# Performance work log

Measured on AMD Instinct MI355X. Metric: run time of the kernel, lower is better.

The kernel has to match this reference:

```python
import jax, jax.numpy as jnp
import numpy as np

P = 16      # patch size
D = 768     # d_model
H = 12      # heads
L = 12      # layers
F = 3072    # d_ff
NC = 1000   # num classes
B = 32
IMG = 224
S = (IMG // P) ** 2 + 1  # 197 tokens (CLS + patches)
EPS = 1e-5


def layernorm(x, s, b):
    m = jnp.mean(x, axis=-1, keepdims=True)
    v = jnp.var(x, axis=-1, keepdims=True)
    return (x - m) * jax.lax.rsqrt(v + EPS) * s + b


def setup_inputs() -> dict:
    key = jax.random.key(0)
    ks = jax.random.split(key, 16)
    sd = 0.02
    patch_dim = P * P * 3  # 768
    inp = {
        "img": jax.random.normal(ks[0], (B, 3, IMG, IMG), jnp.float32),
        "proj_w": jax.random.normal(ks[1], (patch_dim, D), jnp.float32) * sd,
        "proj_b": jnp.zeros((D,), jnp.float32),
        "cls_token": jax.random.normal(ks[2], (1, 1, D), jnp.float32) * sd,
        "pos_emb": jax.random.normal(ks[3], (1, S, D), jnp.float32) * sd,
        # stacked per-layer params [L, ...]
        "ln1_s": jnp.ones((L, D), jnp.float32),
        "ln1_b": jnp.zeros((L, D), jnp.float32),
        "wq": jax.random.normal(ks[4], (L, D, D), jnp.float32) * sd,
        "bq": jnp.zeros((L, D), jnp.float32),
        "wk": jax.random.normal(ks[5], (L, D, D), jnp.float32) * sd,
        "bk": jnp.zeros((L, D), jnp.float32),
        "wv": jax.random.normal(ks[6], (L, D, D), jnp.float32) * sd,
        "bv": jnp.zeros((L, D), jnp.float32),
        "wo": jax.random.normal(ks[7], (L, D, D), jnp.float32) * sd,
        "bo": jnp.zeros((L, D), jnp.float32),
        "ln2_s": jnp.ones((L, D), jnp.float32),
        "ln2_b": jnp.zeros((L, D), jnp.float32),
        "w1": jax.random.normal(ks[8], (L, D, F), jnp.float32) * sd,
        "b1": jnp.zeros((L, F), jnp.float32),
        "w2": jax.random.normal(ks[9], (L, F, D), jnp.float32) * sd,
        "b2": jnp.zeros((L, D), jnp.float32),
        "fnorm_s": jnp.ones((D,), jnp.float32),
        "fnorm_b": jnp.zeros((D,), jnp.float32),
        "head_w": jax.random.normal(ks[10], (D, NC), jnp.float32) * sd,
        "head_b": jnp.zeros((NC,), jnp.float32),
    }
    return inp


def vit_forward(img, proj_w, proj_b, cls_token, pos_emb, ln1_s, ln1_b,
                wq, bq, wk, bk, wv, bv, wo, bo, ln2_s, ln2_b,
                w1, b1, w2, b2, fnorm_s, fnorm_b, head_w, head_b):
    b = img.shape[0]
    g = IMG // P
    # rearrange 'b c (h ph) (w pw) -> b (h w) (ph pw c)'
    x = img.reshape(b, 3, g, P, g, P)
    x = x.transpose(0, 2, 4, 3, 5, 1).reshape(b, g * g, P * P * 3)
    x = x @ proj_w + proj_b                      # [b, 196, D]
    cls = jnp.broadcast_to(cls_token, (b, 1, D))
    x = jnp.concatenate([cls, x], axis=1)        # [b, 197, D]
    x = x + pos_emb                              # learnable positional encoding

    dk = D // H
    scale = 1.0 / jnp.sqrt(jnp.float32(dk))

    def layer(x, p):
        (l1s, l1b, Wq, Bq, Wk, Bk, Wv, Bv, Wo, Bo,
         l2s, l2b, W1, B1, W2, B2) = p
        # pre-norm self-attention with residual
        xn = layernorm(x, l1s, l1b)
        q = (xn @ Wq + Bq).reshape(b, S, H, dk)
        k = (xn @ Wk + Bk).reshape(b, S, H, dk)
        v = (xn @ Wv + Bv).reshape(b, S, H, dk)
        scores = jnp.einsum('bqhd,bkhd->bhqk', q, k) * scale
        attn = jax.nn.softmax(scores, axis=-1)
        ao = jnp.einsum('bhqk,bkhd->bqhd', attn, v).reshape(b, S, D)
        x = x + (ao @ Wo + Bo)
        # pre-norm FFN with residual
        xn = layernorm(x, l2s, l2b)
        h = jax.nn.gelu(xn @ W1 + B1, approximate=False)
        x = x + (h @ W2 + B2)
        return x, None

    params = (ln1_s, ln1_b, wq, bq, wk, bk, wv, bv, wo, bo,
              ln2_s, ln2_b, w1, b1, w2, b2)
    x, _ = jax.lax.scan(layer, x, params)
    x = layernorm(x, fnorm_s, fnorm_b)
    cls_out = x[:, 0, :]
    return cls_out @ head_w + head_b             # [b, num_classes]


def reference(img, proj_w, proj_b, cls_token, pos_emb, ln1_s, ln1_b,
              wq, bq, wk, bk, wv, bv, wo, bo, ln2_s, ln2_b,
              w1, b1, w2, b2, fnorm_s, fnorm_b, head_w, head_b):
    return vit_forward(img, proj_w, proj_b, cls_token, pos_emb, ln1_s, ln1_b,
                       wq, bq, wk, bk, wv, bv, wo, bo, ln2_s, ln2_b,
                       w1, b1, w2, b2, fnorm_s, fnorm_b, head_w, head_b)
```

## Files before the change

kernel.cpp:

```cpp
#include <hip/hip_runtime.h>
#include <stdint.h>

typedef __attribute__((ext_vector_type(4))) float  f32x4;
typedef __attribute__((ext_vector_type(8))) _Float16 f16x8;
typedef __attribute__((ext_vector_type(8))) unsigned short u16x8;

__device__ __forceinline__ unsigned short f2h(float f) {
    _Float16 h = (_Float16)f;
    union { _Float16 h; unsigned short u; } cv; cv.h = h; return cv.u;
}

__device__ __forceinline__ f32x4 mfma16(f16x8 a, f16x8 b, f32x4 c) {
    return __builtin_amdgcn_mfma_f32_16x16x32_f16(a, b, c, 0, 0, 0);
}

__device__ __forceinline__ void async16(const unsigned short* g, unsigned short* l) {
    __builtin_amdgcn_global_load_lds(
        (const __attribute__((address_space(1))) unsigned int*)g,
        (__attribute__((address_space(3))) unsigned int*)l,
        16, 0, 0);
}

template<int EPI, int BK>
__global__ __launch_bounds__(256, (BK == 32 ? 4 : 3))
void gemm_k(const unsigned short* __restrict__ A, const unsigned short* __restrict__ Bw,
            int M, int K, int N,
            float* __restrict__ p0, unsigned short* __restrict__ p1,
            const float* __restrict__ p2, const float* __restrict__ p3,
            unsigned short* __restrict__ p4, unsigned short* __restrict__ p5)
{
    __shared__ unsigned short smem[2 * 64 * BK + 2 * 128 * BK];
    unsigned short (*lA)[64 * BK]  = (unsigned short(*)[64 * BK])smem;
    unsigned short (*lB)[128 * BK] = (unsigned short(*)[128 * BK])(smem + 2 * 64 * BK);
    const int tid  = threadIdx.x;
    const int lane = tid & 63;
    const int wid  = tid >> 6;

    const int gx  = gridDim.x;
    const int nwg = gx * gridDim.y;
    const int lin = blockIdx.y * gx + blockIdx.x;
    const int q = nwg >> 3, r = nwg & 7;
    const int xcd = lin & 7, i = lin >> 3;
    const int wg  = (xcd < r ? xcd * (q + 1) : r * (q + 1) + (xcd - r) * q) + i;
    const int m0 = (wg / gx) * 64;
    const int n0 = (wg % gx) * 128;

    const int colBase = wid * 32;
    const int fr = lane & 15, fg = lane >> 4;

    f32x4 acc[4][2];
#pragma unroll
    for (int a = 0; a < 4; ++a)
#pragma unroll
        for (int b = 0; b < 2; ++b) acc[a][b] = (f32x4){0.f, 0.f, 0.f, 0.f};

    const int nk = K / BK;
    constexpr int CPR = BK / 8;
    constexpr int ACH = 64 * CPR;
    constexpr int NH  = (ACH + 128 * CPR) / 256;

    auto stage = [&](int buf, int kt) {
        const int k0 = kt * BK;
#pragma unroll
        for (int h = 0; h < NH; ++h) {
            const int c = h * 256 + tid;
            const int wbase = h * 256 + wid * 64;
            if (c < ACH) {
                const int row = c / CPR, kc = c % CPR;
                const int gkc = (BK == 32) ? (kc ^ ((row >> 1) & 3)) : (kc ^ (row & 7));
                int ar = m0 + row; if (ar > M - 1) ar = M - 1;
                async16(A + (size_t)ar * K + k0 + gkc * 8,
                        &lA[buf][(size_t)wbase * 8]);
            } else {
                const int cb = c - ACH;
                const int row = cb / CPR, kc = cb % CPR;
                const int gkc = (BK == 32) ? (kc ^ ((row >> 1) & 3)) : (kc ^ (row & 7));
                async16(Bw + (size_t)(n0 + row) * K + k0 + gkc * 8,
                        &lB[buf][(size_t)(wbase - ACH) * 8]);
            }
        }
    };

    stage(0, 0);
    for (int kt = 0; kt < nk; ++kt) {
        __syncthreads();
        if (kt + 1 < nk) stage((kt + 1) & 1, kt + 1);
        const int buf = kt & 1;
#pragma unroll
        for (int kk = 0; kk < BK / 32; ++kk) {
            f16x8 af[4], bfv[2];
#pragma unroll
            for (int mi = 0; mi < 4; ++mi) {
                int row = mi * 16 + fr;
                int pc  = (BK == 32) ? (fg ^ ((row >> 1) & 3))
                                     : ((kk * 4 + fg) ^ (row & 7));
                af[mi] = *(const f16x8*)(&lA[buf][row * BK + pc * 8]);
            }
#pragma unroll
            for (int ni = 0; ni < 2; ++ni) {
                int row = colBase + ni * 16 + fr;
                int pc  = (BK == 32) ? (fg ^ ((row >> 1) & 3))
                                     : ((kk * 4 + fg) ^ (row & 7));
                bfv[ni] = *(const f16x8*)(&lB[buf][row * BK + pc * 8]);
            }
#pragma unroll
            for (int mi = 0; mi < 4; ++mi)
#pragma unroll
                for (int ni = 0; ni < 2; ++ni)
                    acc[mi][ni] = mfma16(af[mi], bfv[ni], acc[mi][ni]);
        }
    }

    const int mat0 = (EPI == 0) ? (n0 / 768) : 0;

    if constexpr (EPI == 0 || EPI == 2) {
        if (EPI == 2 || mat0 < 2) {
            unsigned short* sm = smem;
            __syncthreads();
#pragma unroll
            for (int mi = 0; mi < 4; ++mi)
#pragma unroll
                for (int ni = 0; ni < 2; ++ni) {
                    const int lcol = colBase + ni * 16 + fr;
                    const int colg = n0 + lcol;
#pragma unroll
                    for (int reg = 0; reg < 4; ++reg) {
                        const int lrow = mi * 16 + fg * 4 + reg;
                        float val = acc[mi][ni][reg] + p2[colg];
                        if (EPI == 2)
                            val = 0.5f * val * (1.0f + erff(val * 0.70710678118654752f));
                        sm[lrow * 128 + lcol] = f2h(val);
                    }
                }
            __syncthreads();
#pragma unroll
            for (int it = 0; it < 4; ++it) {
                const int e = it * 256 + tid;
                const int lrow = e >> 4, cch = e & 15;
                const int grow = m0 + lrow;
                if (grow >= M) continue;
                const u16x8 v = *(const u16x8*)(&sm[lrow * 128 + cch * 8]);
                if (EPI == 2) {
                    *(u16x8*)(p1 + (size_t)grow * 3072 + n0 + cch * 8) = v;
                } else {
                    const int colg = n0 + cch * 8;
                    const int w = colg - mat0 * 768;
                    const int h = w >> 6, d = w & 63;
                    const int b = grow / 197, s = grow - b * 197;
                    unsigned short* dst = (mat0 == 0) ? p1 : p4;
                    *(u16x8*)(dst + ((((size_t)b * 12 + h) * 197 + s) * 64 + d)) = v;
                }
            }
        } else {
#pragma unroll
            for (int mi = 0; mi < 4; ++mi)
#pragma unroll
                for (int ni = 0; ni < 2; ++ni) {
                    const int col = n0 + colBase + ni * 16 + fr;
                    const int w = col - 1536;
                    const int h = w >> 6, d = w & 63;
#pragma unroll
                    for (int reg = 0; reg < 4; ++reg) {
                        const int row = m0 + mi * 16 + fg * 4 + reg;
                        if (row >= M) continue;
                        const int b = row / 197, s = row - b * 197;
                        float val = acc[mi][ni][reg] + p2[col];
                        p5[(((size_t)b * 12 + h) * 64 + d) * 208 + s] = f2h(val);
                    }
                }
        }
    } else {
#pragma unroll
        for (int mi = 0; mi < 4; ++mi) {
#pragma unroll
            for (int ni = 0; ni < 2; ++ni) {
                const int col = n0 + colBase + ni * 16 + fr;
#pragma unroll
                for (int reg = 0; reg < 4; ++reg) {
                    const int row = m0 + mi * 16 + fg * 4 + reg;
                    if (row >= M) continue;
                    const float v = acc[mi][ni][reg];
                    if constexpr (EPI == 1 || EPI == 3) {
                        size_t idx = (size_t)row * 768 + col;
                        p0[idx] = p0[idx] + v + p2[col];
                    } else {
                        int b = row / 196, p = row - b * 196;
                        float val = v + p2[col] + p3[(size_t)(1 + p) * 768 + col];
                        p0[((size_t)(b * 197 + 1 + p)) * 768 + col] = val;
                    }
                }
            }
        }
    }
}

__device__ __forceinline__ void convT_body(const float* __restrict__ src,
                                           unsigned short* __restrict__ dst,
                                           int K, int N, int bx, int by,
                                           float (*t)[65])
{
    const int tid = threadIdx.x;
    const int n0 = bx * 64, k0 = by * 64;
    int r = tid >> 4, cq = tid & 15;
#pragma unroll
    for (int i = 0; i < 4; ++i) {
        f32x4 v = *(const f32x4*)(src + (size_t)(k0 + r + i * 16) * N + n0 + cq * 4);
        t[r + i * 16][cq * 4 + 0] = v.x;
        t[r + i * 16][cq * 4 + 1] = v.y;
        t[r + i * 16][cq * 4 + 2] = v.z;
        t[r + i * 16][cq * 4 + 3] = v.w;
    }
    __syncthreads();
    int nl = tid >> 2, kq = tid & 3;
    u16x8 o0, o1;
#pragma unroll
    for (int j = 0; j < 8; ++j) {
        o0[j] = f2h(t[kq * 16 + j][nl]);
        o1[j] = f2h(t[kq * 16 + 8 + j][nl]);
    }
    unsigned short* d = dst + (size_t)(n0 + nl) * K + k0 + kq * 16;
    *(u16x8*)(d)     = o0;
    *(u16x8*)(d + 8) = o1;
}

__device__ __forceinline__ void prep_block(int pid,
            const float* __restrict__ wq, const float* __restrict__ wk,
            const float* __restrict__ wv, const float* __restrict__ wo,
            const float* __restrict__ w1, const float* __restrict__ w2,
            const float* __restrict__ bq, const float* __restrict__ bk,
            const float* __restrict__ bv,
            unsigned short* __restrict__ wqkvT, unsigned short* __restrict__ woT,
            unsigned short* __restrict__ w1T, unsigned short* __restrict__ w2T,
            float* __restrict__ bqkv, float (*t)[65])
{
    if (pid == 1728) {
        for (int c = threadIdx.x; c < 2304; c += 256) {
            int m = c / 768, w = c - m * 768;
            bqkv[c] = (m == 0) ? bq[w] : (m == 1 ? bk[w] : bv[w]);
        }
        return;
    }
    const float* src; unsigned short* dst; int K, N, bx, by;
    if (pid < 576) {
        int mat = pid / 144, r = pid - mat * 144;
        K = 768; N = 768; bx = r % 12; by = r / 12;
        if (mat == 0)      { src = wq; dst = wqkvT; }
        else if (mat == 1) { src = wk; dst = wqkvT + 768ull * 768; }
        else if (mat == 2) { src = wv; dst = wqkvT + 1536ull * 768; }
        else               { src = wo; dst = woT; }
    } else if (pid < 1152) {
        int r = pid - 576; K = 768; N = 3072; bx = r % 48; by = r / 48;
        src = w1; dst = w1T;
    } else {
        int r = pid - 1152; K = 3072; N = 768; bx = r % 12; by = r / 12;
        src = w2; dst = w2T;
    }
    convT_body(src, dst, K, N, bx, by, t);
}

__global__ __launch_bounds__(256)
void prep_k(const float* __restrict__ wq, const float* __restrict__ wk,
            const float* __restrict__ wv, const float* __restrict__ wo,
            const float* __restrict__ w1, const float* __restrict__ w2,
            const float* __restrict__ bq, const float* __restrict__ bk,
            const float* __restrict__ bv,
            unsigned short* __restrict__ wqkvT, unsigned short* __restrict__ woT,
            unsigned short* __restrict__ w1T, unsigned short* __restrict__ w2T,
            float* __restrict__ bqkv)
{
    __shared__ float t[64][65];
    prep_block(blockIdx.x, wq, wk, wv, wo, w1, w2, bq, bk, bv,
               wqkvT, woT, w1T, w2T, bqkv, t);
}

__global__ __launch_bounds__(256, 4)
void attn_prep_k(const unsigned short* __restrict__ qb, const unsigned short* __restrict__ kb,
                 const unsigned short* __restrict__ vt, unsigned short* __restrict__ ao,
                 const float* __restrict__ wq, const float* __restrict__ wk,
                 const float* __restrict__ wv, const float* __restrict__ wo,
                 const float* __restrict__ w1, const float* __restrict__ w2,
                 const float* __restrict__ bq, const float* __restrict__ bk,
                 const float* __restrict__ bv,
                 unsigned short* __restrict__ wqkvT, unsigned short* __restrict__ woT,
                 unsigned short* __restrict__ w1T, unsigned short* __restrict__ w2T,
                 float* __restrict__ bqkv)
{
    __shared__ float smbuf[32 * 210 + 32];

    const int bid = blockIdx.x;
    if (bid >= 2688) {
        prep_block(bid - 2688, wq, wk, wv, wo, w1, w2, bq, bk, bv,
                   wqkvT, woT, w1T, w2T, bqkv,
                   reinterpret_cast<float(*)[65]>(smbuf));
        return;
    }

    float* sc   = smbuf;
    float* rinv = smbuf + 32 * 210;

    const int bh = bid % 384;
    const int qt = bid / 384;
    const int b = bh / 12, h = bh - b * 12;
    const unsigned short* qh  = qb + (size_t)bh * 197 * 64;
    const unsigned short* kh  = kb + (size_t)bh * 197 * 64;
    const unsigned short* vth = vt + (size_t)bh * 64 * 208;
    const int tid = threadIdx.x, lane = tid & 63, wid = tid >> 6;
    const int fr = lane & 15, fg = lane >> 4;

    f16x8 qf[2][2];
#pragma unroll
    for (int mi = 0; mi < 2; ++mi)
#pragma unroll
        for (int kc = 0; kc < 2; ++kc) {
            int s = qt * 32 + mi * 16 + fr; if (s > 196) s = 196;
            qf[mi][kc] = *(const f16x8*)(qh + (size_t)s * 64 + kc * 32 + fg * 8);
        }

    for (int nt = wid; nt < 13; nt += 4) {
        f32x4 a0 = (f32x4){0.f,0.f,0.f,0.f}, a1 = a0;
        int rs = nt * 16 + fr; if (rs > 196) rs = 196;
#pragma unroll
        for (int kc = 0; kc < 2; ++kc) {
            f16x8 kf = *(const f16x8*)(kh + (size_t)rs * 64 + kc * 32 + fg * 8);
            a0 = mfma16(qf[0][kc], kf, a0);
            a1 = mfma16(qf[1][kc], kf, a1);
        }
        int ccol = nt * 16 + fr;
        bool valid = (ccol < 197);
#pragma unroll
        for (int reg = 0; reg < 4; ++reg) {
            int mr = fg * 4 + reg;
            sc[mr * 210 + ccol]        = valid ? a0[reg] * 0.125f : -1e30f;
            sc[(16 + mr) * 210 + ccol] = valid ? a1[reg] * 0.125f : -1e30f;
        }
    }
    __syncthreads();

    {
        int row = tid >> 3, j = tid & 7;
        float m = -1e30f;
        for (int c = j; c < 208; c += 8) m = fmaxf(m, sc[row * 210 + c]);
#pragma unroll
        for (int o = 1; o < 8; o <<= 1) m = fmaxf(m, __shfl_xor(m, o));
        float sum = 0.f;
        for (int c = j; c < 208; c += 8) {
            float e = __expf(sc[row * 210 + c] - m);
            sc[row * 210 + c] = e;
            sum += e;
        }
#pragma unroll
        for (int o = 1; o < 8; o <<= 1) sum += __shfl_xor(sum, o);
        if (j == 0) rinv[row] = 1.0f / sum;
    }
    __syncthreads();

    f32x4 o0 = (f32x4){0.f,0.f,0.f,0.f}, o1 = o0;
    const int dbase = wid * 16;
    for (int kt = 0; kt < 7; ++kt) {
        int kb8 = kt * 32 + fg * 8;
        f16x8 pa0, pa1, vf;
        if (kb8 >= 208) {
#pragma unroll
            for (int j = 0; j < 8; ++j) { pa0[j] = (_Float16)0.f; pa1[j] = (_Float16)0.f; vf[j] = (_Float16)0.f; }
        } else {
            const float* pr0 = &sc[fr * 210 + kb8];
            const float* pr1 = &sc[(16 + fr) * 210 + kb8];
#pragma unroll
            for (int j = 0; j < 8; ++j) { pa0[j] = (_Float16)pr0[j]; pa1[j] = (_Float16)pr1[j]; }
            vf = *(const f16x8*)(vth + (size_t)(dbase + fr) * 208 + kb8);
        }
        o0 = mfma16(pa0, vf, o0);
        o1 = mfma16(pa1, vf, o1);
    }
#pragma unroll
    for (int reg = 0; reg < 4; ++reg) {
        int mr0 = fg * 4 + reg, s0 = qt * 32 + mr0;
        if (s0 < 197)
            ao[((size_t)(b * 197 + s0)) * 768 + h * 64 + dbase + fr] = f2h(o0[reg] * rinv[mr0]);
        int mr1 = 16 + fg * 4 + reg, s1 = qt * 32 + mr1;
        if (s1 < 197)
            ao[((size_t)(b * 197 + s1)) * 768 + h * 64 + dbase + fr] = f2h(o1[reg] * rinv[mr1]);
    }
}

__global__ __launch_bounds__(256, 4)
void ln_k(const float* __restrict__ x, const float* __restrict__ gs,
          const float* __restrict__ gb, unsigned short* __restrict__ out)
{
    const int row = blockIdx.x;
    const int tid = threadIdx.x, lane = tid & 63, wid = tid >> 6;
    const float* xr = x + (size_t)row * 768;
    float v0 = xr[tid], v1 = xr[tid + 256], v2 = xr[tid + 512];
    float s = v0 + v1 + v2;
    float q = v0 * v0 + v1 * v1 + v2 * v2;
#pragma unroll
    for (int o = 1; o < 64; o <<= 1) { s += __shfl_xor(s, o); q += __shfl_xor(q, o); }
    __shared__ float ws[4], wq[4];
    if (lane == 0) { ws[wid] = s; wq[wid] = q; }
    __syncthreads();
    s = ws[0] + ws[1] + ws[2] + ws[3];
    q = wq[0] + wq[1] + wq[2] + wq[3];
    const float mean = s * (1.0f / 768.0f);
    const float rstd = rsqrtf(q * (1.0f / 768.0f) - mean * mean + 1e-5f);
    unsigned short* orow = out + (size_t)row * 768;
    orow[tid]       = f2h((v0 - mean) * rstd * gs[tid]       + gb[tid]);
    orow[tid + 256] = f2h((v1 - mean) * rstd * gs[tid + 256] + gb[tid + 256]);
    orow[tid + 512] = f2h((v2 - mean) * rstd * gs[tid + 512] + gb[tid + 512]);
}

__global__ __launch_bounds__(256)
void convT_k(const float* __restrict__ src, unsigned short* __restrict__ dst, int K, int N)
{
    __shared__ float t[64][65];
    convT_body(src, dst, K, N, blockIdx.x, blockIdx.y, t);
}

__global__ __launch_bounds__(256)
void patch_k(const float* __restrict__ img, unsigned short* __restrict__ patches)
{
    const int t = blockIdx.x;
    const int pxy = threadIdx.x;
    const int b = t / 196, pi = t - b * 196;
    const int gy = pi / 14, gx = pi - gy * 14;
    const int py = pxy >> 4, px = pxy & 15;
    const int yy = gy * 16 + py, xx = gx * 16 + px;
    const float* base = img + ((size_t)b * 3 * 224 + yy) * 224 + xx;
    float c0 = base[0];
    float c1 = base[224 * 224];
    float c2 = base[2 * 224 * 224];
    unsigned short* d = patches + (size_t)t * 768 + pxy * 3;
    d[0] = f2h(c0); d[1] = f2h(c1); d[2] = f2h(c2);
}

__global__ void cls_k(const float* __restrict__ cls, const float* __restrict__ pos,
                      float* __restrict__ x)
{
    int c = blockIdx.x * 256 + threadIdx.x;
    int b = blockIdx.y;
    x[((size_t)b * 197) * 768 + c] = cls[c] + pos[c];
}

__global__ __launch_bounds__(256, 4)
void head_k(const float* __restrict__ x, const float* __restrict__ fs, const float* __restrict__ fb,
            const float* __restrict__ hw, const float* __restrict__ hb, float* __restrict__ out)
{
    __shared__ float xn[768];
    __shared__ float ws[4], wq_[4];
    const int b  = blockIdx.y;
    const int n0 = blockIdx.x * 125;
    const int tid = threadIdx.x, lane = tid & 63, wid = tid >> 6;
    const float* xr = x + (size_t)b * 197 * 768;
    float v0 = xr[tid], v1 = xr[tid + 256], v2 = xr[tid + 512];
    float s = v0 + v1 + v2, q = v0 * v0 + v1 * v1 + v2 * v2;
#pragma unroll
    for (int o = 1; o < 64; o <<= 1) { s += __shfl_xor(s, o); q += __shfl_xor(q, o); }
    if (lane == 0) { ws[wid] = s; wq_[wid] = q; }
    __syncthreads();
    s = ws[0] + ws[1] + ws[2] + ws[3];
    q = wq_[0] + wq_[1] + wq_[2] + wq_[3];
    float mean = s * (1.f / 768.f);
    float rstd = rsqrtf(q * (1.f / 768.f) - mean * mean + 1e-5f);
    xn[tid]       = (v0 - mean) * rstd * fs[tid]       + fb[tid];
    xn[tid + 256] = (v1 - mean) * rstd * fs[tid + 256] + fb[tid + 256];
    xn[tid + 512] = (v2 - mean) * rstd * fs[tid + 512] + fb[tid + 512];
    __syncthreads();

    const int nrel = tid >> 1, half = tid & 1;
    const int n = n0 + nrel;
    float acc = 0.f;
    if (nrel < 125) {
        const float* hp = hw + (size_t)(half * 384) * 1000 + n;
        const float* xp = xn + half * 384;
#pragma unroll 4
        for (int k = 0; k < 384; ++k) acc = fmaf(xp[k], hp[(size_t)k * 1000], acc);
    }
    acc += __shfl_xor(acc, 1);
    if (half == 0 && nrel < 125) out[(size_t)b * 1000 + n] = acc + hb[n];
}

extern "C" void kernel_launch(void* const* d_in, const int* in_sizes, int n_in,
                              void* d_out, int out_size, void* d_ws, size_t ws_size,
                              hipStream_t stream)
{
    (void)in_sizes; (void)n_in; (void)out_size; (void)ws_size;
    const float* img    = (const float*)d_in[0];
    const float* proj_w = (const float*)d_in[1];
    const float* proj_b = (const float*)d_in[2];
    const float* cls_t  = (const float*)d_in[3];
    const float* pos    = (const float*)d_in[4];
    const float* ln1_s  = (const float*)d_in[5];
    const float* ln1_b  = (const float*)d_in[6];
    const float* wq     = (const float*)d_in[7];
    const float* bq     = (const float*)d_in[8];
    const float* wk     = (const float*)d_in[9];
    const float* bk     = (const float*)d_in[10];
    const float* wv     = (const float*)d_in[11];
    const float* bv     = (const float*)d_in[12];
    const float* wo     = (const float*)d_in[13];
    const float* bo     = (const float*)d_in[14];
    const float* ln2_s  = (const float*)d_in[15];
    const float* ln2_b  = (const float*)d_in[16];
    const float* w1     = (const float*)d_in[17];
    const float* b1     = (const float*)d_in[18];
    const float* w2     = (const float*)d_in[19];
    const float* b2     = (const float*)d_in[20];
    const float* fs     = (const float*)d_in[21];
    const float* fb     = (const float*)d_in[22];
    const float* hw     = (const float*)d_in[23];
    const float* hb     = (const float*)d_in[24];

    char* ws = (char*)d_ws;
    size_t off = 0;
    auto alloc = [&](size_t bytes) -> char* {
        char* r = ws + off;
        off += (bytes + 255) & ~(size_t)255;
        return r;
    };
    unsigned short* wqkvT[2]; unsigned short* woT[2];
    unsigned short* w1T[2];   unsigned short* w2T[2];
    float* bqkv[2];
    for (int s = 0; s < 2; ++s) {
        wqkvT[s] = (unsigned short*)alloc(2304ull * 768 * 2);
        woT[s]   = (unsigned short*)alloc(768ull * 768 * 2);
        w1T[s]   = (unsigned short*)alloc(3072ull * 768 * 2);
        w2T[s]   = (unsigned short*)alloc(768ull * 3072 * 2);
        bqkv[s]  = (float*)alloc(2304 * 4);
    }
    unsigned short* projT = (unsigned short*)alloc(768ull * 768 * 2);
    float*          x     = (float*)alloc(6304ull * 768 * 4);
    unsigned short* xn    = (unsigned short*)alloc(6304ull * 768 * 2);
    unsigned short* qbuf  = (unsigned short*)alloc(4841472ull * 2);
    unsigned short* kbuf  = (unsigned short*)alloc(4841472ull * 2);
    unsigned short* vbufT = (unsigned short*)alloc(384ull * 64 * 208 * 2);
    unsigned short* aob   = (unsigned short*)alloc(6304ull * 768 * 2);
    unsigned short* hbuf  = (unsigned short*)alloc(6304ull * 3072 * 2);
    unsigned short* patches = hbuf;

    convT_k<<<dim3(12, 12), 256, 0, stream>>>(proj_w, projT, 768, 768);
    patch_k<<<dim3(6272), 256, 0, stream>>>(img, patches);
    prep_k<<<dim3(1729), 256, 0, stream>>>(
        wq, wk, wv, wo, w1, w2, bq, bk, bv,
        wqkvT[0], woT[0], w1T[0], w2T[0], bqkv[0]);
    gemm_k<4, 32><<<dim3(6, 98), 256, 0, stream>>>(patches, projT, 6272, 768, 768,
                                                   x, nullptr, proj_b, pos, nullptr, nullptr);
    cls_k<<<dim3(3, 32), 256, 0, stream>>>(cls_t, pos, x);

    for (int l = 0; l < 12; ++l) {
        const int set = l & 1, nxt = set ^ 1;
        const int lp  = (l < 11) ? l + 1 : 11;
        const int nprep = (l < 11) ? 1729 : 0;

        ln_k<<<dim3(6304), 256, 0, stream>>>(x, ln1_s + l * 768, ln1_b + l * 768, xn);
        gemm_k<0, 32><<<dim3(18, 99), 256, 0, stream>>>(xn, wqkvT[set], 6304, 768, 2304,
                                                        nullptr, qbuf, bqkv[set], nullptr, kbuf, vbufT);
        attn_prep_k<<<dim3(2688 + nprep), 256, 0, stream>>>(
            qbuf, kbuf, vbufT, aob,
            wq + (size_t)lp * 768 * 768, wk + (size_t)lp * 768 * 768,
            wv + (size_t)lp * 768 * 768, wo + (size_t)lp * 768 * 768,
            w1 + (size_t)lp * 768 * 3072, w2 + (size_t)lp * 3072 * 768,
            bq + lp * 768, bk + lp * 768, bv + lp * 768,
            wqkvT[nxt], woT[nxt], w1T[nxt], w2T[nxt], bqkv[nxt]);
        gemm_k<1, 32><<<dim3(6, 99), 256, 0, stream>>>(aob, woT[set], 6304, 768, 768,
                                                       x, nullptr, bo + l * 768, nullptr, nullptr, nullptr);
        ln_k<<<dim3(6304), 256, 0, stream>>>(x, ln2_s + l * 768, ln2_b + l * 768, xn);
        gemm_k<2, 32><<<dim3(24, 99), 256, 0, stream>>>(xn, w1T[set], 6304, 768, 3072,
                                                        nullptr, hbuf, b1 + l * 3072, nullptr, nullptr, nullptr);
        gemm_k<3, 64><<<dim3(6, 99), 256, 0, stream>>>(hbuf, w2T[set], 6304, 3072, 768,
                                                       x, nullptr, b2 + l * 768, nullptr, nullptr, nullptr);
    }

    head_k<<<dim3(8, 32), 256, 0, stream>>>(x, fs, fb, hw, hb, (float*)d_out);
}
```

Measured before the change: 3.035 ms.

## Load B fragments directly from global into registers, drop B LDS staging

The weight (B) tile is no longer staged through LDS. Each wave loads its own B fragments straight from global memory into registers, double-buffered one k-tile ahead, so LDS holds only the A tile. The smaller LDS footprint lets the launch bounds ask for more resident workgroups, and the epilogue staging buffer gets a padded row stride (136) to reduce bank conflicts. The risks are uncoalesced, non-swizzled global reads for B, more register pressure from the prefetched fragments, and weaker B reuse across waves.

```diff
diff --git a/kernel.cpp b/kernel.cpp
--- a/kernel.cpp
+++ b/kernel.cpp
@@ -22,16 +22,19 @@
 }
 
 template<int EPI, int BK>
-__global__ __launch_bounds__(256, (BK == 32 ? 4 : 3))
+__global__ __launch_bounds__(256, (BK == 32 ? 6 : 4))
 void gemm_k(const unsigned short* __restrict__ A, const unsigned short* __restrict__ Bw,
             int M, int K, int N,
             float* __restrict__ p0, unsigned short* __restrict__ p1,
             const float* __restrict__ p2, const float* __restrict__ p3,
             unsigned short* __restrict__ p4, unsigned short* __restrict__ p5)
 {
-    __shared__ unsigned short smem[2 * 64 * BK + 2 * 128 * BK];
-    unsigned short (*lA)[64 * BK]  = (unsigned short(*)[64 * BK])smem;
-    unsigned short (*lB)[128 * BK] = (unsigned short(*)[128 * BK])(smem + 2 * 64 * BK);
+    constexpr int SMSTG = 2 * 64 * BK;
+    constexpr int SMU   = (EPI == 0 || EPI == 2)
+                          ? (SMSTG > 64 * 136 ? SMSTG : 64 * 136)
+                          : SMSTG;
+    __shared__ unsigned short smem[SMU];
+    unsigned short (*lA)[64 * BK] = (unsigned short(*)[64 * BK])smem;
     const int tid  = threadIdx.x;
     const int lane = tid & 63;
     const int wid  = tid >> 6;
@@ -56,39 +59,41 @@
 
     const int nk = K / BK;
     constexpr int CPR = BK / 8;
-    constexpr int ACH = 64 * CPR;
-    constexpr int NH  = (ACH + 128 * CPR) / 256;
-
-    auto stage = [&](int buf, int kt) {
+    constexpr int NHA = (64 * CPR) / 256;
+
+    auto stageA = [&](int buf, int kt) {
         const int k0 = kt * BK;
 #pragma unroll
-        for (int h = 0; h < NH; ++h) {
+        for (int h = 0; h < NHA; ++h) {
             const int c = h * 256 + tid;
-            const int wbase = h * 256 + wid * 64;
-            if (c < ACH) {
-                const int row = c / CPR, kc = c % CPR;
-                const int gkc = (BK == 32) ? (kc ^ ((row >> 1) & 3)) : (kc ^ (row & 7));
-                int ar = m0 + row; if (ar > M - 1) ar = M - 1;
-                async16(A + (size_t)ar * K + k0 + gkc * 8,
-                        &lA[buf][(size_t)wbase * 8]);
-            } else {
-                const int cb = c - ACH;
-                const int row = cb / CPR, kc = cb % CPR;
-                const int gkc = (BK == 32) ? (kc ^ ((row >> 1) & 3)) : (kc ^ (row & 7));
-                async16(Bw + (size_t)(n0 + row) * K + k0 + gkc * 8,
-                        &lB[buf][(size_t)(wbase - ACH) * 8]);
+            const int row = c / CPR, kc = c % CPR;
+            const int gkc = (BK == 32) ? (kc ^ ((row >> 1) & 3)) : (kc ^ (row & 7));
+            int ar = m0 + row; if (ar > M - 1) ar = M - 1;
+            async16(A + (size_t)ar * K + k0 + gkc * 8,
+                    &lA[buf][(size_t)(h * 256 + wid * 64) * 8]);
+        }
+    };
+    auto loadB = [&](int kt, f16x8 (&dst)[BK / 32][2]) {
+        const int k0 = kt * BK;
+#pragma unroll
+        for (int kk = 0; kk < BK / 32; ++kk)
+#pragma unroll
+            for (int ni = 0; ni < 2; ++ni) {
+                const int row = n0 + colBase + ni * 16 + fr;
+                dst[kk][ni] = *(const f16x8*)(Bw + (size_t)row * K + k0 + kk * 32 + fg * 8);
             }
-        }
     };
 
-    stage(0, 0);
+    f16x8 bcur[BK / 32][2], bnxt[BK / 32][2];
+    stageA(0, 0);
+    loadB(0, bcur);
     for (int kt = 0; kt < nk; ++kt) {
         __syncthreads();
-        if (kt + 1 < nk) stage((kt + 1) & 1, kt + 1);
+        if (kt + 1 < nk) { stageA((kt + 1) & 1, kt + 1); loadB(kt + 1, bnxt); }
         const int buf = kt & 1;
 #pragma unroll
         for (int kk = 0; kk < BK / 32; ++kk) {
-            f16x8 af[4], bfv[2];
+            f16x8 af[4];
 #pragma unroll
             for (int mi = 0; mi < 4; ++mi) {
                 int row = mi * 16 + fr;
@@ -97,17 +102,16 @@
                 af[mi] = *(const f16x8*)(&lA[buf][row * BK + pc * 8]);
             }
 #pragma unroll
-            for (int ni = 0; ni < 2; ++ni) {
-                int row = colBase + ni * 16 + fr;
-                int pc  = (BK == 32) ? (fg ^ ((row >> 1) & 3))
-                                     : ((kk * 4 + fg) ^ (row & 7));
-                bfv[ni] = *(const f16x8*)(&lB[buf][row * BK + pc * 8]);
-            }
-#pragma unroll
             for (int mi = 0; mi < 4; ++mi)
 #pragma unroll
                 for (int ni = 0; ni < 2; ++ni)
-                    acc[mi][ni] = mfma16(af[mi], bfv[ni], acc[mi][ni]);
+                    acc[mi][ni] = mfma16(af[mi], bcur[kk][ni], acc[mi][ni]);
+        }
+        if (kt + 1 < nk) {
+#pragma unroll
+            for (int kk = 0; kk < BK / 32; ++kk)
+#pragma unroll
+                for (int ni = 0; ni < 2; ++ni) bcur[kk][ni] = bnxt[kk][ni];
         }
     }
 
@@ -129,7 +133,7 @@
                         float val = acc[mi][ni][reg] + p2[colg];
                         if (EPI == 2)
                             val = 0.5f * val * (1.0f + erff(val * 0.70710678118654752f));
-                        sm[lrow * 128 + lcol] = f2h(val);
+                        sm[lrow * 136 + lcol] = f2h(val);
                     }
                 }
             __syncthreads();
@@ -139,7 +143,7 @@
                 const int lrow = e >> 4, cch = e & 15;
                 const int grow = m0 + lrow;
                 if (grow >= M) continue;
-                const u16x8 v = *(const u16x8*)(&sm[lrow * 128 + cch * 8]);
+                const u16x8 v = *(const u16x8*)(&sm[lrow * 136 + cch * 8]);
                 if (EPI == 2) {
                     *(u16x8*)(p1 + (size_t)grow * 3072 + n0 + cch * 8) = v;
                 } else {
```

Result: slower. 3.792 ms (+25.0%).
